# Performance work log

Hardware: AMD Instinct MI355X
Metric: run time of the kernel (lower is better)

## Reference

```python
import jax, jax.numpy as jnp
import numpy as np

BETA = 0.25

def setup_inputs() -> dict:
    key = jax.random.key(0)
    k1, k2 = jax.random.split(key)
    z = jax.random.normal(k1, (32, 256, 32, 32), dtype=jnp.float32)
    # embedding init ~ U(-1/K, 1/K) as intended by the module
    K, D = 1024, 256
    codebook = jax.random.uniform(k2, (K, D), dtype=jnp.float32, minval=-1.0 / K, maxval=1.0 / K)
    return {"z": z, "codebook": codebook}


def reference(z, codebook):
    # z: [B, D, H, W] -> [B, H, W, D]
    zt = jnp.transpose(z, (0, 2, 3, 1))
    B, H, W, D = zt.shape
    z_flat = zt.reshape(-1, D)  # [N, D]
    # pairwise squared distance: ||z||^2 + ||e||^2 - 2 z e^T
    dist = (
        jnp.sum(z_flat * z_flat, axis=1, keepdims=True)
        + jnp.sum(codebook * codebook, axis=1)[None, :]
        - 2.0 * jnp.matmul(z_flat, codebook.T)
    )  # [N, K]
    idx = jnp.argmin(dist, axis=1)  # [N]
    z_q = codebook[idx].reshape(B, H, W, D)
    sg = jax.lax.stop_gradient
    loss = jnp.mean((sg(z_q) - zt) ** 2) + BETA * jnp.mean((sg(zt) - z_q) ** 2)
    # straight-through estimator
    z_q = zt + sg(z_q - zt)
    z_q = jnp.transpose(z_q, (0, 3, 1, 2))  # back to [B, D, H, W]
    return z_q, idx, loss
```

## Files before the change

kernel.cpp:

```cpp
#include <hip/hip_runtime.h>


#define D_DIM   256
#define K_CODES 1024
#define HW      1024
#define MT      128
#define NT      256
#define BK      8
#define THREADS 512
#define NSTEP   128

#define ZQ_OFF   0
#define IDX_OFF  8388608
#define LOSS_OFF 8421376

#define SMEM_FLOATS (D_DIM*MT + 2*BK*NT + MT + MT)
#define SMEM_BYTES  (SMEM_FLOATS * 4)

extern __shared__ float smem[];

__global__ void enorm_kernel(const float* __restrict__ cb, float* __restrict__ enorm) {
    int gt = blockIdx.x * blockDim.x + threadIdx.x;
    int k = gt >> 6;
    int lane = gt & 63;
    const float4* row = (const float4*)(cb + (size_t)k * D_DIM);
    float4 v = row[lane];
    float s = fmaf(v.x, v.x, fmaf(v.y, v.y, fmaf(v.z, v.z, v.w * v.w)));
    #pragma unroll
    for (int off = 32; off; off >>= 1) s += __shfl_xor(s, off);
    if (lane == 0) enorm[k] = s;
}

__global__ __launch_bounds__(THREADS, 2) void vq_kernel(
        const float* __restrict__ z, const float* __restrict__ cb,
        const float* __restrict__ enorm, float* __restrict__ out)
{
    float* As = smem;
    float* Es = smem + D_DIM * MT;
    int*   bestm   = (int*)(smem + D_DIM*MT + 2*BK*NT);
    float* znorm_s = (float*)(smem + D_DIM*MT + 2*BK*NT + MT);

    const int t   = threadIdx.x;
    const int blk = blockIdx.x;
    const int b   = blk >> 3;
    const int p0  = (blk & 7) * MT;
    const float* zb = z + (size_t)b * D_DIM * HW;

    for (int i = t; i < D_DIM * MT / 4; i += THREADS) {
        int d = i >> 5, m4 = i & 31;
        *(float4*)(As + d * MT + m4 * 4) = *(const float4*)(zb + d * HW + p0 + m4 * 4);
    }
    __syncthreads();

    {
        int m = t & (MT - 1), q = t >> 7;
        const float* col = As + m;
        double zp = 0.0;
        #pragma unroll 8
        for (int d = q * 64; d < q * 64 + 64; ++d) {
            double v = (double)col[d * MT];
            zp += v * v;
        }
        double* zscr = (double*)Es;
        zscr[q * MT + m] = zp;
    }
    __syncthreads();
    if (t < MT) {
        double* zscr = (double*)Es;
        double s = (zscr[t] + zscr[MT + t]) + (zscr[2 * MT + t] + zscr[3 * MT + t]);
        znorm_s[t] = (float)s;
    }
    __syncthreads();

    const int tx = t & 31, ty = t >> 5;
    const int m_base = ty * 8;
    const int kx4 = tx * 4;

    float znf[8];
    #pragma unroll
    for (int i = 0; i < 8; ++i) znf[i] = znorm_s[m_base + i];

    float bestv[8]; int besti[8];
    #pragma unroll
    for (int i = 0; i < 8; ++i) { bestv[i] = 3.4e38f; besti[i] = 0; }

    const int skk = t >> 1, sd4 = t & 1;
    const float* cbp = cb + (size_t)skk * D_DIM + sd4 * 4;

    {
        float4 v = *(const float4*)(cbp);
        Es[(sd4 * 4 + 0) * NT + skk] = v.x;
        Es[(sd4 * 4 + 1) * NT + skk] = v.y;
        Es[(sd4 * 4 + 2) * NT + skk] = v.z;
        Es[(sd4 * 4 + 3) * NT + skk] = v.w;
    }
    __syncthreads();

    int cur = 0;
    for (int c = 0; c < 4; ++c) {
        const int k0 = c * NT;
        float acc[8][8];
        #pragma unroll
        for (int i = 0; i < 8; ++i)
            #pragma unroll
            for (int j = 0; j < 8; ++j) acc[i][j] = 0.f;

        for (int s = 0; s < 32; ++s) {
            const int g = c * 32 + s;
            const bool more = (g + 1 < NSTEP);
            float4 sv;
            if (more) {
                const int gn = g + 1;
                sv = *(const float4*)(cbp + (((size_t)(gn >> 5)) << 16) + ((gn & 31) << 3));
            }

            const float* Ec = Es + cur * (BK * NT);
            const int dk = s * BK;
            #pragma unroll
            for (int dd = 0; dd < BK; ++dd) {
                float a[8], e[8];
                *(float4*)(a)     = *(const float4*)(As + (dk + dd) * MT + m_base);
                *(float4*)(a + 4) = *(const float4*)(As + (dk + dd) * MT + m_base + 4);
                *(float4*)(e)     = *(const float4*)(Ec + dd * NT + kx4);
                *(float4*)(e + 4) = *(const float4*)(Ec + dd * NT + 128 + kx4);
                #pragma unroll
                for (int i = 0; i < 8; ++i)
                    #pragma unroll
                    for (int j = 0; j < 8; ++j)
                        acc[i][j] = fmaf(a[i], e[j], acc[i][j]);
            }

            if (more) {
                float* En = Es + (cur ^ 1) * (BK * NT);
                En[(sd4 * 4 + 0) * NT + skk] = sv.x;
                En[(sd4 * 4 + 1) * NT + skk] = sv.y;
                En[(sd4 * 4 + 2) * NT + skk] = sv.z;
                En[(sd4 * 4 + 3) * NT + skk] = sv.w;
            }
            __syncthreads();
            cur ^= 1;
        }

        #pragma unroll
        for (int j = 0; j < 8; ++j) {
            const int kidx = k0 + ((j < 4) ? (kx4 + j) : (124 + kx4 + j));
            const float bn = enorm[kidx];
            #pragma unroll
            for (int i = 0; i < 8; ++i) {
                float A   = znf[i] + bn;
                float val = A - 2.0f * acc[i][j];
                if (val < bestv[i] || (val == bestv[i] && kidx < besti[i])) {
                    bestv[i] = val; besti[i] = kidx;
                }
            }
        }
    }

    #pragma unroll
    for (int i = 0; i < 8; ++i) {
        float v = bestv[i]; int ix = besti[i];
        #pragma unroll
        for (int off = 16; off; off >>= 1) {
            float ov = __shfl_xor(v, off);
            int   oi = __shfl_xor(ix, off);
            if (ov < v || (ov == v && oi < ix)) { v = ov; ix = oi; }
        }
        if (tx == 0) {
            bestm[m_base + i] = ix;
            out[IDX_OFF + (size_t)blk * MT + m_base + i] = (float)ix;
        }
    }
    __syncthreads();

    float lsum = 0.f;
    const size_t zq_base = (size_t)b * D_DIM * HW + p0;
    for (int i2 = t; i2 < D_DIM * MT / 4; i2 += THREADS) {
        int p = i2 & (MT - 1), d4 = i2 >> 7;
        int idx = bestm[p];
        float4 cv = *(const float4*)(cb + (size_t)idx * D_DIM + d4 * 4);
        float z0 = As[(d4 * 4 + 0) * MT + p];
        float z1 = As[(d4 * 4 + 1) * MT + p];
        float z2 = As[(d4 * 4 + 2) * MT + p];
        float z3 = As[(d4 * 4 + 3) * MT + p];
        float e0 = cv.x - z0, e1 = cv.y - z1, e2 = cv.z - z2, e3 = cv.w - z3;
        lsum = fmaf(e0, e0, lsum); lsum = fmaf(e1, e1, lsum);
        lsum = fmaf(e2, e2, lsum); lsum = fmaf(e3, e3, lsum);
        out[zq_base + (size_t)(d4 * 4 + 0) * HW + p] = cv.x;
        out[zq_base + (size_t)(d4 * 4 + 1) * HW + p] = cv.y;
        out[zq_base + (size_t)(d4 * 4 + 2) * HW + p] = cv.z;
        out[zq_base + (size_t)(d4 * 4 + 3) * HW + p] = cv.w;
    }
    #pragma unroll
    for (int off = 32; off; off >>= 1) lsum += __shfl_xor(lsum, off);
    __syncthreads();
    if ((t & 63) == 0) Es[t >> 6] = lsum;
    __syncthreads();
    if (t == 0) {
        float s = 0.f;
        #pragma unroll
        for (int w = 0; w < 8; ++w) s += Es[w];
        atomicAdd(out + LOSS_OFF, s * (1.25f / 8388608.f));
    }
}

extern "C" void kernel_launch(void* const* d_in, const int* in_sizes, int n_in,
                              void* d_out, int out_size, void* d_ws, size_t ws_size,
                              hipStream_t stream) {
    const float* z  = (const float*)d_in[0];
    const float* cb = (const float*)d_in[1];
    float* out = (float*)d_out;
    float* enorm = (float*)d_ws;

    hipMemsetAsync(out + LOSS_OFF, 0, sizeof(float), stream);

    enorm_kernel<<<256, 256, 0, stream>>>(cb, enorm);

    hipFuncSetAttribute((const void*)vq_kernel,
                        hipFuncAttributeMaxDynamicSharedMemorySize, SMEM_BYTES);
    vq_kernel<<<256, THREADS, SMEM_BYTES, stream>>>(z, cb, enorm, out);
}
```

Baseline: 295.5 us.

## Widen codebook tile to 512 with 16x8 per-thread microtile

Changes the per-thread register tile from 8x8 to 16x8 and the codebook tile width from 256 to 512 codes with a K-step of 4. Each thread now loads one codebook row slice directly, so staging needs no strided split. The loop runs two chunks of 64 steps instead of four chunks of 32. The larger microtile raises FMA work per shared-memory load but adds register pressure under launch_bounds(512,2), risking spills or lower occupancy. It also doubles the number of barriers per reduction depth.

```diff
diff --git a/kernel.cpp b/kernel.cpp
--- a/kernel.cpp
+++ b/kernel.cpp
@@ -5,8 +5,8 @@
 #define K_CODES 1024
 #define HW      1024
 #define MT      128
-#define NT      256
-#define BK      8
+#define NT      512
+#define BK      4
 #define THREADS 512
 #define NSTEP   128
 
@@ -72,59 +72,57 @@
     }
     __syncthreads();
 
-    const int tx = t & 31, ty = t >> 5;
-    const int m_base = ty * 8;
+    const int tx = t & 63;
+    const int m_base = (t >> 6) * 16;
     const int kx4 = tx * 4;
 
-    float znf[8];
-    #pragma unroll
-    for (int i = 0; i < 8; ++i) znf[i] = znorm_s[m_base + i];
-
-    float bestv[8]; int besti[8];
-    #pragma unroll
-    for (int i = 0; i < 8; ++i) { bestv[i] = 3.4e38f; besti[i] = 0; }
-
-    const int skk = t >> 1, sd4 = t & 1;
-    const float* cbp = cb + (size_t)skk * D_DIM + sd4 * 4;
+    float bestv[16]; int besti[16];
+    #pragma unroll
+    for (int i = 0; i < 16; ++i) { bestv[i] = 3.4e38f; besti[i] = 0; }
+
+    const float* cbp = cb + (size_t)t * D_DIM;
 
     {
         float4 v = *(const float4*)(cbp);
-        Es[(sd4 * 4 + 0) * NT + skk] = v.x;
-        Es[(sd4 * 4 + 1) * NT + skk] = v.y;
-        Es[(sd4 * 4 + 2) * NT + skk] = v.z;
-        Es[(sd4 * 4 + 3) * NT + skk] = v.w;
+        Es[0 * NT + t] = v.x;
+        Es[1 * NT + t] = v.y;
+        Es[2 * NT + t] = v.z;
+        Es[3 * NT + t] = v.w;
     }
     __syncthreads();
 
     int cur = 0;
-    for (int c = 0; c < 4; ++c) {
-        const int k0 = c * NT;
-        float acc[8][8];
-        #pragma unroll
-        for (int i = 0; i < 8; ++i)
+    for (int c = 0; c < 2; ++c) {
+        float acc[16][8];
+        #pragma unroll
+        for (int i = 0; i < 16; ++i)
             #pragma unroll
             for (int j = 0; j < 8; ++j) acc[i][j] = 0.f;
 
-        for (int s = 0; s < 32; ++s) {
-            const int g = c * 32 + s;
+        for (int s = 0; s < 64; ++s) {
+            const int g = c * 64 + s;
             const bool more = (g + 1 < NSTEP);
             float4 sv;
             if (more) {
                 const int gn = g + 1;
-                sv = *(const float4*)(cbp + (((size_t)(gn >> 5)) << 16) + ((gn & 31) << 3));
+                sv = *(const float4*)(cbp + (((size_t)(gn >> 6)) << 17) + ((gn & 63) << 2));
             }
 
             const float* Ec = Es + cur * (BK * NT);
             const int dk = s * BK;
             #pragma unroll
             for (int dd = 0; dd < BK; ++dd) {
-                float a[8], e[8];
-                *(float4*)(a)     = *(const float4*)(As + (dk + dd) * MT + m_base);
-                *(float4*)(a + 4) = *(const float4*)(As + (dk + dd) * MT + m_base + 4);
-                *(float4*)(e)     = *(const float4*)(Ec + dd * NT + kx4);
-                *(float4*)(e + 4) = *(const float4*)(Ec + dd * NT + 128 + kx4);
+                const float* Ar = As + (dk + dd) * MT + m_base;
+                float a[16], e[8];
+                *(float4*)(a)      = *(const float4*)(Ar);
+                *(float4*)(a + 4)  = *(const float4*)(Ar + 4);
+                *(float4*)(a + 8)  = *(const float4*)(Ar + 8);
+                *(float4*)(a + 12) = *(const float4*)(Ar + 12);
+                const float* Er = Ec + dd * NT + kx4;
+                *(float4*)(e)     = *(const float4*)(Er);
+                *(float4*)(e + 4) = *(const float4*)(Er + 256);
                 #pragma unroll
-                for (int i = 0; i < 8; ++i)
+                for (int i = 0; i < 16; ++i)
                     #pragma unroll
                     for (int j = 0; j < 8; ++j)
                         acc[i][j] = fmaf(a[i], e[j], acc[i][j]);
@@ -132,10 +130,10 @@
 
             if (more) {
                 float* En = Es + (cur ^ 1) * (BK * NT);
-                En[(sd4 * 4 + 0) * NT + skk] = sv.x;
-                En[(sd4 * 4 + 1) * NT + skk] = sv.y;
-                En[(sd4 * 4 + 2) * NT + skk] = sv.z;
-                En[(sd4 * 4 + 3) * NT + skk] = sv.w;
+                En[0 * NT + t] = sv.x;
+                En[1 * NT + t] = sv.y;
+                En[2 * NT + t] = sv.z;
+                En[3 * NT + t] = sv.w;
             }
             __syncthreads();
             cur ^= 1;
@@ -143,11 +141,11 @@
 
         #pragma unroll
         for (int j = 0; j < 8; ++j) {
-            const int kidx = k0 + ((j < 4) ? (kx4 + j) : (124 + kx4 + j));
+            const int kidx = c * NT + ((j < 4) ? (kx4 + j) : (252 + kx4 + j));
             const float bn = enorm[kidx];
             #pragma unroll
-            for (int i = 0; i < 8; ++i) {
-                float A   = znf[i] + bn;
+            for (int i = 0; i < 16; ++i) {
+                float A   = znorm_s[m_base + i] + bn;
                 float val = A - 2.0f * acc[i][j];
                 if (val < bestv[i] || (val == bestv[i] && kidx < besti[i])) {
                     bestv[i] = val; besti[i] = kidx;
@@ -157,10 +155,10 @@
     }
 
     #pragma unroll
-    for (int i = 0; i < 8; ++i) {
+    for (int i = 0; i < 16; ++i) {
         float v = bestv[i]; int ix = besti[i];
         #pragma unroll
-        for (int off = 16; off; off >>= 1) {
+        for (int off = 32; off; off >>= 1) {
             float ov = __shfl_xor(v, off);
             int   oi = __shfl_xor(ix, off);
             if (ov < v || (ov == v && oi < ix)) { v = ov; ix = oi; }
```

After: 328.8 us. 1.11x slower.
